# Optimization experiments

Hardware: AMD Instinct MI355X
Metric: run time of the kernel (lower is better)

## Reference

```python
import jax, jax.numpy as jnp
import numpy as np

B, S, H = 2, 2048, 1024
NH, DH = 16, 64  # num heads, head dim

def setup_inputs() -> dict:
    key = jax.random.key(0)
    ks = jax.random.split(key, 4)
    scale = 0.02
    return {
        "hidden_states": jax.random.normal(ks[0], (B, S, H), dtype=jnp.float32),
        "attention_mask": jnp.zeros((B, 1, 1, S), dtype=jnp.float32),  # additive mask
        "Wq": jax.random.normal(ks[1], (H, H), dtype=jnp.float32) * scale,
        "bq": jnp.zeros((H,), dtype=jnp.float32),
        "Wk": jax.random.normal(ks[2], (H, H), dtype=jnp.float32) * scale,
        "bk": jnp.zeros((H,), dtype=jnp.float32),
        "Wv": jax.random.normal(ks[3], (H, H), dtype=jnp.float32) * scale,
        "bv": jnp.zeros((H,), dtype=jnp.float32),
    }

def _split_heads(x):
    # [B,S,H] -> [B,NH,S,DH]
    return x.reshape(B, S, NH, DH).transpose(0, 2, 1, 3)

def reference(hidden_states, attention_mask, Wq, bq, Wk, bk, Wv, bv):
    q = _split_heads(hidden_states @ Wq + bq)
    k = _split_heads(hidden_states @ Wk + bk)
    v = _split_heads(hidden_states @ Wv + bv)
    # scores: [B,NH,S,S]
    scores = jnp.einsum('bhqd,bhkd->bhqk', q, k) / jnp.asarray(np.sqrt(DH), scores_dtype := q.dtype)
    scores = scores + attention_mask  # additive mask broadcast
    probs = jax.nn.softmax(scores, axis=-1)
    out = jnp.einsum('bhqk,bhkd->bhqd', probs, v)  # [B,NH,S,DH]
    out = out.transpose(0, 2, 1, 3).reshape(B, S, H)
    return out
```

## Files before the change

kernel.cpp:

```cpp
#include <hip/hip_runtime.h>
#include <hip/hip_bf16.h>

#define Bn  2
#define Sn  2048
#define Hn  1024
#define NHn 16
#define DHn 64
#define Mn  (Bn * Sn)

typedef __attribute__((ext_vector_type(4)))  float    f32x4;
typedef __attribute__((ext_vector_type(16))) float    f32x16;
typedef __attribute__((ext_vector_type(8)))  _Float16 h8;
typedef __attribute__((ext_vector_type(4)))  _Float16 h4;
typedef __attribute__((ext_vector_type(2)))  __fp16   fp16x2;
typedef __attribute__((ext_vector_type(2)))  unsigned int u32x2;

union H2PK { fp16x2 v; unsigned int u; };
union U4H8 { unsigned int u[4]; h8 v; };

#define MFMA16F(a, b, c) __builtin_amdgcn_mfma_f32_16x16x32_f16(a, b, c, 0, 0, 0)
#define MFMA32F(a, b, c) __builtin_amdgcn_mfma_f32_32x32x16_f16(a, b, c, 0, 0, 0)

#define SCFULL 0.18033688011112042f
#define L2E    1.44269504088896340736f

__device__ __forceinline__ void glds16(const void* g, void* l) {
    __builtin_amdgcn_global_load_lds(
        (const __attribute__((address_space(1))) unsigned int*)g,
        (__attribute__((address_space(3))) unsigned int*)l, 16, 0, 0);
}

__global__ __launch_bounds__(256) void prep(
    const float* __restrict__ X, const float* __restrict__ W0,
    const float* __restrict__ W1, const float* __restrict__ W2,
    const float* __restrict__ Msk,
    _Float16* __restrict__ Xh, _Float16* __restrict__ WT,
    _Float16* __restrict__ Wm)
{
    const int bid = blockIdx.x;
    const int tid = threadIdx.x;
    __shared__ float Ws[64][65];

    if (bid < 4096) {
        const int i = bid * 256 + tid;
        float4 x = ((const float4*)X)[i];
        h4 o;
        o[0] = (_Float16)x.x; o[1] = (_Float16)x.y;
        o[2] = (_Float16)x.z; o[3] = (_Float16)x.w;
        *(h4*)&Xh[(size_t)i * 4] = o;
        return;
    }
    if (bid >= 4096 + 768) {
#pragma unroll
        for (int it = 0; it < 16; ++it) {
            const int idx = it * 256 + tid;
            Wm[idx] = (_Float16)__builtin_amdgcn_exp2f(Msk[idx] * L2E);
        }
        return;
    }

    const int wb = bid - 4096;
    const int which = wb >> 8;
    const int rem = wb & 255;
    const int k0 = ((rem >> 4) & 15) * 64;
    const int n0 = (rem & 15) * 64;
    const float* W = (which == 0) ? W0 : (which == 1 ? W1 : W2);
    _Float16* O = WT + (size_t)which * Hn * Hn;

#pragma unroll
    for (int it = 0; it < 4; ++it) {
        const int idx = tid + 256 * it;
        const int row = idx >> 4, c4 = (idx & 15) * 4;
        float4 w = *(const float4*)&W[(size_t)(k0 + row) * Hn + n0 + c4];
        Ws[row][c4 + 0] = w.x; Ws[row][c4 + 1] = w.y;
        Ws[row][c4 + 2] = w.z; Ws[row][c4 + 3] = w.w;
    }
    __syncthreads();
#pragma unroll
    for (int it = 0; it < 16; ++it) {
        const int e = tid + 256 * it;
        const int k = e & 63, n = e >> 6;
        O[(size_t)(n0 + n) * Hn + k0 + k] = (_Float16)Ws[k][n];
    }
}

__global__ __launch_bounds__(256) void qkv_mfma(
    const _Float16* __restrict__ Xh, const _Float16* __restrict__ WTA,
    const float* __restrict__ b0, const float* __restrict__ b1,
    const float* __restrict__ b2, const _Float16* __restrict__ Wm,
    _Float16* __restrict__ Qh, _Float16* __restrict__ Kh,
    _Float16* __restrict__ VTh)
{
    const int which = blockIdx.z;
    const _Float16* WT = WTA + (size_t)which * Hn * Hn;
    const float* bias = (which == 0) ? b0 : (which == 1 ? b1 : b2);
    _Float16* Dst = (which == 0) ? Qh : (which == 1 ? Kh : VTh);

    const int m0 = blockIdx.x * 128;
    const int n0 = blockIdx.y * 128;
    const int tid  = threadIdx.x;
    const int wid  = tid >> 6;
    const int lane = tid & 63;
    const int l16  = lane & 15;
    const int quad = lane >> 4;
    const int wm = wid >> 1, wn = wid & 1;

    __shared__ _Float16 Ah[128 * 64], Bh[128 * 64];

    f32x4 acc[4][4];
#pragma unroll
    for (int i = 0; i < 4; ++i)
#pragma unroll
        for (int j = 0; j < 4; ++j) acc[i][j] = (f32x4){0.f, 0.f, 0.f, 0.f};

    for (int kt = 0; kt < Hn / 64; ++kt) {
        const int k0 = kt * 64;
        __syncthreads();
#pragma unroll
        for (int c = 0; c < 4; ++c) {
            const int idx = (wid * 4 + c) * 64 + lane;
            const int row = idx >> 3;
            const int cg  = (idx & 7) ^ (row & 7);
            glds16(&Xh[(size_t)(m0 + row) * Hn + k0 + cg * 8],
                   &Ah[(wid * 4 + c) * 512]);
            glds16(&WT[(size_t)(n0 + row) * Hn + k0 + cg * 8],
                   &Bh[(wid * 4 + c) * 512]);
        }
        __syncthreads();

#pragma unroll
        for (int kk = 0; kk < 2; ++kk) {
            h8 xa[4], wb[4];
#pragma unroll
            for (int t = 0; t < 4; ++t) {
                const int ar = wm * 64 + t * 16 + l16;
                const int br = wn * 64 + t * 16 + l16;
                xa[t] = *(const h8*)&Ah[ar * 64 + (((kk * 4 + quad) ^ (ar & 7)) * 8)];
                wb[t] = *(const h8*)&Bh[br * 64 + (((kk * 4 + quad) ^ (br & 7)) * 8)];
            }
            if (which < 2) {
#pragma unroll
                for (int i = 0; i < 4; ++i)
#pragma unroll
                    for (int j = 0; j < 4; ++j)
                        acc[i][j] = MFMA16F(xa[i], wb[j], acc[i][j]);
            } else {
#pragma unroll
                for (int i = 0; i < 4; ++i)
#pragma unroll
                    for (int j = 0; j < 4; ++j)
                        acc[i][j] = MFMA16F(wb[i], xa[j], acc[i][j]);
            }
        }
    }

    const float oscale = (which == 0) ? SCFULL : 1.0f;
    if (which < 2) {
#pragma unroll
        for (int j = 0; j < 4; ++j) {
            const int n = n0 + wn * 64 + j * 16 + l16;
            const float bv = bias[n];
            const int hh = n >> 6, dd = n & 63;
#pragma unroll
            for (int i = 0; i < 4; ++i) {
                const int mb = m0 + wm * 64 + i * 16 + quad * 4;
#pragma unroll
                for (int r = 0; r < 4; ++r) {
                    const int m = mb + r;
                    const int b = m >> 11, s = m & (Sn - 1);
                    Dst[(((size_t)b * NHn + hh) * Sn + s) * DHn + dd] =
                        (_Float16)((acc[i][j][r] + bv) * oscale);
                }
            }
        }
    } else {
        float wvj[4];
#pragma unroll
        for (int j = 0; j < 4; ++j)
            wvj[j] = (float)Wm[m0 + wm * 64 + j * 16 + l16];
#pragma unroll
        for (int i = 0; i < 4; ++i) {
#pragma unroll
            for (int r = 0; r < 4; ++r) {
                const int n = n0 + wn * 64 + i * 16 + quad * 4 + r;
                const float bv = bias[n];
                const int hh = n >> 6, dd = n & 63;
#pragma unroll
                for (int j = 0; j < 4; ++j) {
                    const int m = m0 + wm * 64 + j * 16 + l16;
                    const int b = m >> 11, s = m & (Sn - 1);
                    Dst[(((size_t)b * NHn + hh) * DHn + dd) * Sn + s] =
                        (_Float16)((acc[i][j][r] + bv) * wvj[j]);
                }
            }
        }
    }
}

__global__ __launch_bounds__(256, 2) void attn(
    const _Float16* __restrict__ Qh, const _Float16* __restrict__ Kh,
    const _Float16* __restrict__ VTh, const _Float16* __restrict__ Wmg,
    float* __restrict__ Out)
{
    const int flat = blockIdx.x + 16 * blockIdx.y + 256 * blockIdx.z;
    const int bh   = ((flat & 7) << 2) | ((flat >> 3) & 3);
    const int qb   = flat >> 5;
    const int b = bh >> 4, h = bh & 15;

    const int tid  = threadIdx.x;
    const int wid  = tid >> 6;
    const int lane = tid & 63;
    const int l32  = lane & 31;
    const int hi   = lane >> 5;

    __shared__ __align__(16) _Float16 Kb[4][4096];
    __shared__ __align__(16) _Float16 Vb[4][4096];
    __shared__ __align__(16) _Float16 Wb[4][512];

    const int q0 = qb * 128 + wid * 32;

    const size_t qbase = ((size_t)bh * Sn + q0 + l32) * DHn;
    h8 qf[4];
#pragma unroll
    for (int kd = 0; kd < 4; ++kd)
        qf[kd] = *(const h8*)&Qh[qbase + kd * 16 + hi * 8];

    asm volatile("s_waitcnt vmcnt(0)" ::: "memory");

    const _Float16* Kg = Kh  + (size_t)bh * Sn * DHn;
    const _Float16* Vg = VTh + (size_t)bh * DHn * Sn;
    const _Float16* Wg = Wmg + (size_t)b * Sn;

    auto stage = [&](int kt, int buf) {
        const int koff = kt * 64;
#pragma unroll
        for (int c = 0; c < 2; ++c) {
            const int idx = (wid * 2 + c) * 64 + lane;
            const int row = idx >> 3;
            const int cg  = (idx & 7) ^ (row & 7);
            glds16(&Kg[(size_t)(koff + row) * DHn + cg * 8],
                   &Kb[buf][(wid * 2 + c) * 512]);
            glds16(&Vg[(size_t)row * Sn + koff + cg * 8],
                   &Vb[buf][(wid * 2 + c) * 512]);
        }
        glds16(&Wg[koff + lane * 8], &Wb[buf][0]);
    };

    stage(0, 0);
    stage(1, 1);

    f32x16 sA[2], sB[2], o[2], acc_l;
#pragma unroll
    for (int dt = 0; dt < 2; ++dt) o[dt] = (f32x16)(0.f);
    acc_l = (f32x16)(0.f);

    auto qkt = [&](f32x16 (&s)[2], int buf) {
        __builtin_amdgcn_s_setprio(1);
#pragma unroll
        for (int t = 0; t < 2; ++t) {
            f32x16 c = (f32x16)(0.f);
#pragma unroll
            for (int kd = 0; kd < 4; ++kd) {
                const int row = t * 32 + l32;
                h8 kf = *(const h8*)&Kb[buf][row * 64 +
                                             (((kd * 2 + hi) ^ (row & 7)) * 8)];
                c = MFMA32F(kf, qf[kd], c);
            }
            s[t] = c;
        }
        __builtin_amdgcn_s_setprio(0);
    };

    auto sm_pv = [&](f32x16 (&s)[2], int buf) {
        unsigned int pk[2][4][2];
#pragma unroll
        for (int t = 0; t < 2; ++t) {
#pragma unroll
            for (int g = 0; g < 4; ++g) {
                const float p0 = __builtin_amdgcn_exp2f(s[t][g * 4 + 0]);
                const float p1 = __builtin_amdgcn_exp2f(s[t][g * 4 + 1]);
                const float p2 = __builtin_amdgcn_exp2f(s[t][g * 4 + 2]);
                const float p3 = __builtin_amdgcn_exp2f(s[t][g * 4 + 3]);
                H2PK u0, u1;
                u0.v = __builtin_amdgcn_cvt_pkrtz(p0, p1);
                u1.v = __builtin_amdgcn_cvt_pkrtz(p2, p3);
                pk[t][g][0] = u0.u;
                pk[t][g][1] = u1.u;
            }
        }

        __builtin_amdgcn_s_setprio(1);
#pragma unroll
        for (int ks = 0; ks < 4; ++ks) {
            const int t = ks >> 1, ge = (ks & 1) * 2;
            u32x2 rA = __builtin_amdgcn_permlane32_swap(
                pk[t][ge][0], pk[t][ge + 1][0], false, false);
            u32x2 rB = __builtin_amdgcn_permlane32_swap(
                pk[t][ge][1], pk[t][ge + 1][1], false, false);
            U4H8 w;
            w.u[0] = rA[0]; w.u[1] = rB[0]; w.u[2] = rA[1]; w.u[3] = rB[1];
            h8 wv8 = *(const h8*)&Wb[buf][ks * 16 + hi * 8];
            acc_l = MFMA32F(w.v, wv8, acc_l);
#pragma unroll
            for (int dt = 0; dt < 2; ++dt) {
                const int row = dt * 32 + l32;
                h8 vf = *(const h8*)&Vb[buf][row * 64 +
                                             (((ks * 2 + hi) ^ (row & 7)) * 8)];
                o[dt] = MFMA32F(w.v, vf, o[dt]);
            }
        }
        __builtin_amdgcn_s_setprio(0);
    };

    asm volatile("s_waitcnt vmcnt(5)" ::: "memory");
    __builtin_amdgcn_s_barrier();
    qkt(sA, 0);

    auto iter = [&](int kt, f32x16 (&scur)[2], f32x16 (&snxt)[2]) {
        stage(kt + 2, (kt + 2) & 3);
        asm volatile("s_waitcnt vmcnt(5)" ::: "memory");
        __builtin_amdgcn_s_barrier();
        qkt(snxt, (kt + 1) & 3);
        sm_pv(scur, kt & 3);
    };

    for (int kt = 0; kt < 30; kt += 2) {
        iter(kt,     sA, sB);
        iter(kt + 1, sB, sA);
    }
    asm volatile("s_waitcnt vmcnt(0)" ::: "memory");
    __builtin_amdgcn_s_barrier();
    qkt(sB, 31 & 3);
    sm_pv(sA, 30 & 3);
    sm_pv(sB, 31 & 3);

#pragma unroll
    for (int g2 = 0; g2 < 4; ++g2) {
#pragma unroll
        for (int e = 0; e < 4; ++e) {
            const int r = g2 * 4 + e;
            const int q = q0 + 4 * hi + 8 * g2 + e;
            const size_t ob = ((size_t)b * Sn + q) * Hn + h * DHn;
            const float sc = 1.0f / acc_l[r];
#pragma unroll
            for (int dt = 0; dt < 2; ++dt)
                Out[ob + dt * 32 + l32] = o[dt][r] * sc;
        }
    }
}

extern "C" void kernel_launch(void* const* d_in, const int* in_sizes, int n_in,
                              void* d_out, int out_size, void* d_ws, size_t ws_size,
                              hipStream_t stream) {
    const float* X    = (const float*)d_in[0];
    const float* mask = (const float*)d_in[1];
    const float* Wq   = (const float*)d_in[2];
    const float* bq   = (const float*)d_in[3];
    const float* Wk   = (const float*)d_in[4];
    const float* bk   = (const float*)d_in[5];
    const float* Wv   = (const float*)d_in[6];
    const float* bv   = (const float*)d_in[7];
    float* out = (float*)d_out;

    const size_t NE = (size_t)Mn * Hn;
    _Float16* Xh  = (_Float16*)d_ws;
    _Float16* WT  = Xh + NE;
    _Float16* Qh  = WT + (size_t)3 * Hn * Hn;
    _Float16* Kh  = Qh + NE;
    _Float16* VTh = Kh + NE;
    _Float16* Wm  = VTh + NE;

    prep<<<dim3(4096 + 768 + 1), dim3(256), 0, stream>>>(
        X, Wq, Wk, Wv, mask, Xh, WT, Wm);

    dim3 g1(Mn / 128, Hn / 128, 3), b1(256);
    qkv_mfma<<<g1, b1, 0, stream>>>(Xh, WT, bq, bk, bv, Wm, Qh, Kh, VTh);

    dim3 g2(Sn / 128, NHn, Bn), b2(256);
    attn<<<g2, b2, 0, stream>>>(Qh, Kh, VTh, Wm, out);
}
```

Before: 171.2 us.

## Split attention KV tiles across wave pairs with 64-query blocks and LDS reduction

Result: slower. 177.9 us (+3.9%).

```diff
diff --git a/kernel.cpp b/kernel.cpp
--- a/kernel.cpp
+++ b/kernel.cpp
@@ -197,12 +197,12 @@
     }
 }
 
-__global__ __launch_bounds__(256, 2) void attn(
+__global__ __launch_bounds__(256, 3) void attn(
     const _Float16* __restrict__ Qh, const _Float16* __restrict__ Kh,
     const _Float16* __restrict__ VTh, const _Float16* __restrict__ Wmg,
     float* __restrict__ Out)
 {
-    const int flat = blockIdx.x + 16 * blockIdx.y + 256 * blockIdx.z;
+    const int flat = blockIdx.x + 32 * blockIdx.y + 512 * blockIdx.z;
     const int bh   = ((flat & 7) << 2) | ((flat >> 3) & 3);
     const int qb   = flat >> 5;
     const int b = bh >> 4, h = bh & 15;
@@ -212,12 +212,14 @@
     const int lane = tid & 63;
     const int l32  = lane & 31;
     const int hi   = lane >> 5;
-
-    __shared__ __align__(16) _Float16 Kb[4][4096];
-    __shared__ __align__(16) _Float16 Vb[4][4096];
-    __shared__ __align__(16) _Float16 Wb[4][512];
-
-    const int q0 = qb * 128 + wid * 32;
+    const int qsub = wid & 1;
+    const int kh   = wid >> 1;
+
+    __shared__ __align__(16) _Float16 Kb[3][4096];
+    __shared__ __align__(16) _Float16 Vb[3][4096];
+    __shared__ __align__(16) _Float16 Wb[3][512];
+
+    const int q0 = qb * 64 + qsub * 32;
 
     const size_t qbase = ((size_t)bh * Sn + q0 + l32) * DHn;
     h8 qf[4];
@@ -249,63 +251,57 @@
     stage(0, 0);
     stage(1, 1);
 
-    f32x16 sA[2], sB[2], o[2], acc_l;
+    f32x16 sA, sB, o[2], acc_l;
 #pragma unroll
     for (int dt = 0; dt < 2; ++dt) o[dt] = (f32x16)(0.f);
     acc_l = (f32x16)(0.f);
 
-    auto qkt = [&](f32x16 (&s)[2], int buf) {
+    auto qkt = [&](f32x16& s, int buf) {
         __builtin_amdgcn_s_setprio(1);
-#pragma unroll
-        for (int t = 0; t < 2; ++t) {
-            f32x16 c = (f32x16)(0.f);
-#pragma unroll
-            for (int kd = 0; kd < 4; ++kd) {
-                const int row = t * 32 + l32;
-                h8 kf = *(const h8*)&Kb[buf][row * 64 +
-                                             (((kd * 2 + hi) ^ (row & 7)) * 8)];
-                c = MFMA32F(kf, qf[kd], c);
-            }
-            s[t] = c;
-        }
+        f32x16 c = (f32x16)(0.f);
+#pragma unroll
+        for (int kd = 0; kd < 4; ++kd) {
+            const int row = kh * 32 + l32;
+            h8 kf = *(const h8*)&Kb[buf][row * 64 +
+                                         (((kd * 2 + hi) ^ (row & 7)) * 8)];
+            c = MFMA32F(kf, qf[kd], c);
+        }
+        s = c;
         __builtin_amdgcn_s_setprio(0);
     };
 
-    auto sm_pv = [&](f32x16 (&s)[2], int buf) {
-        unsigned int pk[2][4][2];
-#pragma unroll
-        for (int t = 0; t < 2; ++t) {
-#pragma unroll
-            for (int g = 0; g < 4; ++g) {
-                const float p0 = __builtin_amdgcn_exp2f(s[t][g * 4 + 0]);
-                const float p1 = __builtin_amdgcn_exp2f(s[t][g * 4 + 1]);
-                const float p2 = __builtin_amdgcn_exp2f(s[t][g * 4 + 2]);
-                const float p3 = __builtin_amdgcn_exp2f(s[t][g * 4 + 3]);
-                H2PK u0, u1;
-                u0.v = __builtin_amdgcn_cvt_pkrtz(p0, p1);
-                u1.v = __builtin_amdgcn_cvt_pkrtz(p2, p3);
-                pk[t][g][0] = u0.u;
-                pk[t][g][1] = u1.u;
-            }
+    auto sm_pv = [&](f32x16& s, int buf) {
+        unsigned int pk[4][2];
+#pragma unroll
+        for (int g = 0; g < 4; ++g) {
+            const float p0 = __builtin_amdgcn_exp2f(s[g * 4 + 0]);
+            const float p1 = __builtin_amdgcn_exp2f(s[g * 4 + 1]);
+            const float p2 = __builtin_amdgcn_exp2f(s[g * 4 + 2]);
+            const float p3 = __builtin_amdgcn_exp2f(s[g * 4 + 3]);
+            H2PK u0, u1;
+            u0.v = __builtin_amdgcn_cvt_pkrtz(p0, p1);
+            u1.v = __builtin_amdgcn_cvt_pkrtz(p2, p3);
+            pk[g][0] = u0.u;
+            pk[g][1] = u1.u;
         }
 
         __builtin_amdgcn_s_setprio(1);
 #pragma unroll
-        for (int ks = 0; ks < 4; ++ks) {
-            const int t = ks >> 1, ge = (ks & 1) * 2;
+        for (int ks = 0; ks < 2; ++ks) {
+            const int ge = ks * 2;
             u32x2 rA = __builtin_amdgcn_permlane32_swap(
-                pk[t][ge][0], pk[t][ge + 1][0], false, false);
+                pk[ge][0], pk[ge + 1][0], false, false);
             u32x2 rB = __builtin_amdgcn_permlane32_swap(
-                pk[t][ge][1], pk[t][ge + 1][1], false, false);
+                pk[ge][1], pk[ge + 1][1], false, false);
             U4H8 w;
             w.u[0] = rA[0]; w.u[1] = rB[0]; w.u[2] = rA[1]; w.u[3] = rB[1];
-            h8 wv8 = *(const h8*)&Wb[buf][ks * 16 + hi * 8];
+            h8 wv8 = *(const h8*)&Wb[buf][kh * 32 + ks * 16 + hi * 8];
             acc_l = MFMA32F(w.v, wv8, acc_l);
 #pragma unroll
             for (int dt = 0; dt < 2; ++dt) {
                 const int row = dt * 32 + l32;
                 h8 vf = *(const h8*)&Vb[buf][row * 64 +
-                                             (((ks * 2 + hi) ^ (row & 7)) * 8)];
+                           (((kh * 4 + ks * 2 + hi) ^ (row & 7)) * 8)];
                 o[dt] = MFMA32F(w.v, vf, o[dt]);
             }
         }
@@ -314,14 +310,18 @@
 
     asm volatile("s_waitcnt vmcnt(5)" ::: "memory");
     __builtin_amdgcn_s_barrier();
+    asm volatile("" ::: "memory");
     qkt(sA, 0);
 
-    auto iter = [&](int kt, f32x16 (&scur)[2], f32x16 (&snxt)[2]) {
-        stage(kt + 2, (kt + 2) & 3);
-        asm volatile("s_waitcnt vmcnt(5)" ::: "memory");
+    int bc = 0, bn = 1, bs = 2;
+    auto iter = [&](int kt, f32x16& scur, f32x16& snxt) {
+        asm volatile("s_waitcnt vmcnt(0)" ::: "memory");
         __builtin_amdgcn_s_barrier();
-        qkt(snxt, (kt + 1) & 3);
-        sm_pv(scur, kt & 3);
+        asm volatile("" ::: "memory");
+        if (kt + 2 < Sn / 64) stage(kt + 2, bs);
+        qkt(snxt, bn);
+        sm_pv(scur, bc);
+        const int t = bc; bc = bn; bn = bs; bs = t;
     };
 
     for (int kt = 0; kt < 30; kt += 2) {
@@ -330,21 +330,37 @@
     }
     asm volatile("s_waitcnt vmcnt(0)" ::: "memory");
     __builtin_amdgcn_s_barrier();
-    qkt(sB, 31 & 3);
-    sm_pv(sA, 30 & 3);
-    sm_pv(sB, 31 & 3);
-
-#pragma unroll
-    for (int g2 = 0; g2 < 4; ++g2) {
-#pragma unroll
-        for (int e = 0; e < 4; ++e) {
-            const int r = g2 * 4 + e;
-            const int q = q0 + 4 * hi + 8 * g2 + e;
-            const size_t ob = ((size_t)b * Sn + q) * Hn + h * DHn;
-            const float sc = 1.0f / acc_l[r];
-#pragma unroll
-            for (int dt = 0; dt < 2; ++dt)
-                Out[ob + dt * 32 + l32] = o[dt][r] * sc;
+    asm volatile("" ::: "memory");
+    qkt(sB, bn);
+    sm_pv(sA, bc);
+    sm_pv(sB, bn);
+
+    __syncthreads();
+    float* scr = (float*)&Kb[0][0];
+    if (wid >= 2) {
+        float* p = scr + ((size_t)(wid - 2) * 64 + lane) * 48;
+#pragma unroll
+        for (int i = 0; i < 16; ++i) p[i]      = o[0][i];
+#pragma unroll
+        for (int i = 0; i < 16; ++i) p[16 + i] = o[1][i];
+#pragma unroll
+        for (int i = 0; i < 16; ++i) p[32 + i] = acc_l[i];
+    }
+    __syncthreads();
+    if (wid < 2) {
+        const float* p = scr + ((size_t)qsub * 64 + lane) * 48;
+#pragma unroll
+        for (int g2 = 0; g2 < 4; ++g2) {
+#pragma unroll
+            for (int e = 0; e < 4; ++e) {
+                const int r = g2 * 4 + e;
+                const int q = q0 + 4 * hi + 8 * g2 + e;
+                const size_t ob = ((size_t)b * Sn + q) * Hn + h * DHn;
+                const float sc = 1.0f / (acc_l[r] + p[32 + r]);
+#pragma unroll
+                for (int dt = 0; dt < 2; ++dt)
+                    Out[ob + dt * 32 + l32] = (o[dt][r] + p[dt * 16 + r]) * sc;
+            }
         }
     }
 }
@@ -376,6 +392,6 @@
     dim3 g1(Mn / 128, Hn / 128, 3), b1(256);
     qkv_mfma<<<g1, b1, 0, stream>>>(Xh, WT, bq, bk, bv, Wm, Qh, Kh, VTh);
 
-    dim3 g2(Sn / 128, NHn, Bn), b2(256);
+    dim3 g2(Sn / 64, NHn, Bn), b2(256);
     attn<<<g2, b2, 0, stream>>>(Qh, Kh, VTh, Wm, out);
 }
```

## Load K tiles directly into registers instead of staging through LDS

Applied to the files above, without the earlier changes.

Result: slower. 192.5 us (+12.4%).

```diff
diff --git a/kernel.cpp b/kernel.cpp
--- a/kernel.cpp
+++ b/kernel.cpp
@@ -213,7 +213,6 @@
     const int l32  = lane & 31;
     const int hi   = lane >> 5;
 
-    __shared__ __align__(16) _Float16 Kb[4][4096];
     __shared__ __align__(16) _Float16 Vb[4][4096];
     __shared__ __align__(16) _Float16 Wb[4][512];
 
@@ -238,34 +237,39 @@
             const int idx = (wid * 2 + c) * 64 + lane;
             const int row = idx >> 3;
             const int cg  = (idx & 7) ^ (row & 7);
-            glds16(&Kg[(size_t)(koff + row) * DHn + cg * 8],
-                   &Kb[buf][(wid * 2 + c) * 512]);
             glds16(&Vg[(size_t)row * Sn + koff + cg * 8],
                    &Vb[buf][(wid * 2 + c) * 512]);
         }
         glds16(&Wg[koff + lane * 8], &Wb[buf][0]);
     };
 
-    stage(0, 0);
-    stage(1, 1);
+    auto kload = [&](h8 (&kf)[8], int kt) {
+        const int koff = kt * 64;
+#pragma unroll
+        for (int t = 0; t < 2; ++t)
+#pragma unroll
+            for (int kd = 0; kd < 4; ++kd)
+                kf[t * 4 + kd] = *(const h8*)&Kg[
+                    (size_t)(koff + t * 32 + l32) * DHn + kd * 16 + hi * 8];
+    };
+
+    h8 kfA[8], kfB[8];
+    stage(0, 0); kload(kfA, 0);
+    stage(1, 1); kload(kfB, 1);
 
     f32x16 sA[2], sB[2], o[2], acc_l;
 #pragma unroll
     for (int dt = 0; dt < 2; ++dt) o[dt] = (f32x16)(0.f);
     acc_l = (f32x16)(0.f);
 
-    auto qkt = [&](f32x16 (&s)[2], int buf) {
+    auto qkt = [&](f32x16 (&s)[2], const h8 (&kf)[8]) {
         __builtin_amdgcn_s_setprio(1);
 #pragma unroll
         for (int t = 0; t < 2; ++t) {
             f32x16 c = (f32x16)(0.f);
 #pragma unroll
-            for (int kd = 0; kd < 4; ++kd) {
-                const int row = t * 32 + l32;
-                h8 kf = *(const h8*)&Kb[buf][row * 64 +
-                                             (((kd * 2 + hi) ^ (row & 7)) * 8)];
-                c = MFMA32F(kf, qf[kd], c);
-            }
+            for (int kd = 0; kd < 4; ++kd)
+                c = MFMA32F(kf[t * 4 + kd], qf[kd], c);
             s[t] = c;
         }
         __builtin_amdgcn_s_setprio(0);
@@ -312,25 +316,32 @@
         __builtin_amdgcn_s_setprio(0);
     };
 
-    asm volatile("s_waitcnt vmcnt(5)" ::: "memory");
+    asm volatile("s_waitcnt vmcnt(11)" ::: "memory");
     __builtin_amdgcn_s_barrier();
-    qkt(sA, 0);
-
-    auto iter = [&](int kt, f32x16 (&scur)[2], f32x16 (&snxt)[2]) {
+    asm volatile("" ::: "memory");
+    qkt(sA, kfA);
+
+    for (int kt = 0; kt < 30; kt += 2) {
         stage(kt + 2, (kt + 2) & 3);
-        asm volatile("s_waitcnt vmcnt(5)" ::: "memory");
+        kload(kfA, kt + 2);
+        asm volatile("s_waitcnt vmcnt(11)" ::: "memory");
         __builtin_amdgcn_s_barrier();
-        qkt(snxt, (kt + 1) & 3);
-        sm_pv(scur, kt & 3);
-    };
-
-    for (int kt = 0; kt < 30; kt += 2) {
-        iter(kt,     sA, sB);
-        iter(kt + 1, sB, sA);
+        asm volatile("" ::: "memory");
+        qkt(sB, kfB);
+        sm_pv(sA, kt & 3);
+
+        stage(kt + 3, (kt + 3) & 3);
+        kload(kfB, kt + 3);
+        asm volatile("s_waitcnt vmcnt(11)" ::: "memory");
+        __builtin_amdgcn_s_barrier();
+        asm volatile("" ::: "memory");
+        qkt(sA, kfA);
+        sm_pv(sB, (kt + 1) & 3);
     }
     asm volatile("s_waitcnt vmcnt(0)" ::: "memory");
     __builtin_amdgcn_s_barrier();
-    qkt(sB, 31 & 3);
+    asm volatile("" ::: "memory");
+    qkt(sB, kfB);
     sm_pv(sA, 30 & 3);
     sm_pv(sB, 31 & 3);
 
```
